# Kernel tuning notes

Measured on AMD Instinct MI355X. Metric: run time of the kernel, lower is better.

The kernel has to match this reference:

```python
import jax, jax.numpy as jnp
import numpy as np

DIM = 1536
HEADS = 12
HD = DIM // HEADS  # 128
EPS = 1e-6
SINK_SIZE = 1          # frames
MAX_ATTN = 1920        # tokens (sliding window)


def setup_inputs() -> dict:
    key = jax.random.key(0)
    ks = jax.random.split(key, 10)
    B = 1
    F, H, W = 8, 16, 24
    L = F * H * W  # 3072
    s = 0.02
    inp = {
        "x": jax.random.normal(ks[0], (B, L, DIM), jnp.float32),
        "seq_lens": jnp.array([L], jnp.int32),
        "grid_sizes": jnp.array([[F, H, W]], jnp.int32),
        "freqs": jax.random.normal(ks[1], (1024, HD // 2, 2), jnp.float32),
        "wq": jax.random.normal(ks[2], (DIM, DIM), jnp.float32) * s,
        "bq": jnp.zeros((DIM,), jnp.float32),
        "wk": jax.random.normal(ks[3], (DIM, DIM), jnp.float32) * s,
        "bk": jnp.zeros((DIM,), jnp.float32),
        "wv": jax.random.normal(ks[4], (DIM, DIM), jnp.float32) * s,
        "bv": jnp.zeros((DIM,), jnp.float32),
        "wo": jax.random.normal(ks[5], (DIM, DIM), jnp.float32) * s,
        "bo": jnp.zeros((DIM,), jnp.float32),
        "nq_w": jnp.ones((DIM,), jnp.float32),
        "nk_w": jnp.ones((DIM,), jnp.float32),
    }
    return inp


def _rmsnorm(x, w):
    # WanRMSNorm: x * rsqrt(mean(x^2) + eps) * weight
    return x * jax.lax.rsqrt(jnp.mean(x * x, axis=-1, keepdims=True) + EPS) * w


def _rope(x, F, H, W, fc):
    # x: [B, L, n, d]; fc: complex [1024, d//2]
    B, L, n, d = x.shape
    c = d // 2
    c1 = c - 2 * (c // 3)  # temporal split
    c2 = c // 3
    f0, f1, f2 = fc[:, :c1], fc[:, c1:c1 + c2], fc[:, c1 + c2:]
    fr = jnp.concatenate([
        jnp.broadcast_to(f0[:F, None, None, :], (F, H, W, c1)),
        jnp.broadcast_to(f1[None, :H, None, :], (F, H, W, c2)),
        jnp.broadcast_to(f2[None, None, :W, :], (F, H, W, c2)),
    ], axis=-1).reshape(L, 1, c)  # [L, 1, c]
    xp = x.reshape(B, L, n, c, 2)
    xc = jax.lax.complex(xp[..., 0], xp[..., 1])  # [B, L, n, c]
    xr = xc * fr[None]
    return jnp.stack([jnp.real(xr), jnp.imag(xr)], axis=-1).reshape(B, L, n, d)


def reference(x, seq_lens, grid_sizes, freqs, wq, bq, wk, bk, wv, bv, wo, bo, nq_w, nk_w):
    B, L, _ = x.shape
    gs = np.asarray(grid_sizes)[0]
    F, H, W = int(gs[0]), int(gs[1]), int(gs[2])
    fs = H * W  # frame_seqlen
    sink = SINK_SIZE * fs

    q = _rmsnorm(x @ wq.T + bq, nq_w).reshape(B, L, HEADS, HD)
    k = _rmsnorm(x @ wk.T + bk, nk_w).reshape(B, L, HEADS, HD)
    v = (x @ wv.T + bv).reshape(B, L, HEADS, HD)

    fc = jax.lax.complex(freqs[..., 0], freqs[..., 1])  # [1024, HD//2]
    q = _rope(q, F, H, W, fc)
    k = _rope(k, F, H, W, fc)

    # sink + windowed frame-causal block mask (flex_attention block_mask)
    idx = jnp.arange(L)
    qf = idx // fs
    kf = idx // fs
    mask = (kf[None, :] <= qf[:, None]) & (
        (idx[None, :] < sink) | (idx[None, :] >= (qf[:, None] + 1) * fs - MAX_ATTN)
    )  # [L, L]

    scale = 1.0 / np.float32(np.sqrt(HD))
    scores = jnp.einsum('bqnd,bknd->bnqk', q, k) * scale
    scores = jnp.where(mask[None, None], scores, jnp.float32(-1e30))
    attn = jax.nn.softmax(scores, axis=-1)
    out = jnp.einsum('bnqk,bknd->bqnd', attn, v).reshape(B, L, DIM)
    return out @ wo.T + bo
```

## Files before the change

kernel.cpp:

```cpp
#include <hip/hip_runtime.h>
#include <stdint.h>

#define DIMC 1536
#define LTOK 3072
#define HEADS 12
#define HD 128
#define FS 384
#define MAXATTN 1920
#define HTOK 1152
#define NHT 1920

typedef __attribute__((ext_vector_type(4))) float f32x4;
typedef __attribute__((ext_vector_type(8))) short bf16x8;

__device__ __forceinline__ unsigned short f2bf(float f) {
  union { float f; unsigned int u; } c; c.f = f;
  unsigned int u = c.u + 0x7fffu + ((c.u >> 16) & 1u);
  return (unsigned short)(u >> 16);
}
__device__ __forceinline__ float bf2f(unsigned short s) {
  union { unsigned int u; float f; } c; c.u = (unsigned int)s << 16; return c.f;
}

__device__ __forceinline__ void dma16(const void* g, void* l) {
  __builtin_amdgcn_global_load_lds(
      (const __attribute__((address_space(1))) unsigned int*)g,
      (__attribute__((address_space(3))) unsigned int*)l, 16, 0, 0);
}

__global__ __launch_bounds__(256)
void cvt_all_k(const float* __restrict__ x, const float* __restrict__ wq,
               const float* __restrict__ wk, const float* __restrict__ wv,
               const float* __restrict__ wo,
               unsigned short* __restrict__ xb, unsigned short* __restrict__ wqb,
               unsigned short* __restrict__ wkb, unsigned short* __restrict__ wvb,
               unsigned short* __restrict__ wob)
{
  const int i = blockIdx.x * 256 + threadIdx.x;
  const int n0 = LTOK * DIMC / 4;
  const int nw = DIMC * DIMC / 4;
  const float* src; unsigned short* dst; int off;
  if (i < n0) { src = x; dst = xb; off = i; }
  else {
    int j = i - n0; int w = j / nw; off = j - w * nw;
    src = (w == 0) ? wq : (w == 1) ? wk : (w == 2) ? wv : wo;
    dst = (w == 0) ? wqb : (w == 1) ? wkb : (w == 2) ? wvb : wob;
  }
  float4 f = ((const float4*)src)[off];
  uint2 o;
  o.x = (unsigned int)f2bf(f.x) | ((unsigned int)f2bf(f.y) << 16);
  o.y = (unsigned int)f2bf(f.z) | ((unsigned int)f2bf(f.w) << 16);
  ((uint2*)dst)[off] = o;
}

template <bool F32OUT>
__global__ __launch_bounds__(256)
void gemm_nt(const unsigned short* __restrict__ A,
             const unsigned short* __restrict__ B0,
             const unsigned short* __restrict__ B1,
             const unsigned short* __restrict__ B2,
             const float* __restrict__ bias0,
             const float* __restrict__ bias1,
             const float* __restrict__ bias2,
             void* __restrict__ o0, void* __restrict__ o1, void* __restrict__ o2)
{
  const int z = blockIdx.z;
  const unsigned short* Bw = (z == 0) ? B0 : (z == 1) ? B1 : B2;
  const float* bias = (z == 0) ? bias0 : (z == 1) ? bias1 : bias2;
  void* outp = (z == 0) ? o0 : (z == 1) ? o1 : o2;

  __shared__ __align__(16) unsigned short lA[128 * 32];
  __shared__ __align__(16) unsigned short lB[128 * 32];

  const int tid = threadIdx.x;
  const int wave = tid >> 6;
  const int lane = tid & 63;
  const int m0 = blockIdx.y * 128;
  const int n0 = blockIdx.x * 128;
  const int wm = (wave >> 1) * 64;
  const int wn = (wave & 1) * 64;

  f32x4 acc[4][4] = {};

  const int srow = tid >> 2;
  const int scol = (tid & 3) * 8;
  const int fr = lane & 15;
  const int fk = (lane >> 4) * 8;

  unsigned short* la0 = &lA[srow * 32 + scol];
  unsigned short* la1 = &lA[(srow + 64) * 32 + scol];
  unsigned short* lb0 = &lB[srow * 32 + scol];
  unsigned short* lb1 = &lB[(srow + 64) * 32 + scol];
  const unsigned short* ga0 = A  + (size_t)(m0 + srow)      * DIMC + scol;
  const unsigned short* ga1 = A  + (size_t)(m0 + srow + 64) * DIMC + scol;
  const unsigned short* gb0 = Bw + (size_t)(n0 + srow)      * DIMC + scol;
  const unsigned short* gb1 = Bw + (size_t)(n0 + srow + 64) * DIMC + scol;

  for (int k0 = 0; k0 < DIMC; k0 += 32) {
    dma16(ga0 + k0, la0);
    dma16(ga1 + k0, la1);
    dma16(gb0 + k0, lb0);
    dma16(gb1 + k0, lb1);
    __syncthreads();

    bf16x8 af[4], bf[4];
#pragma unroll
    for (int i = 0; i < 4; ++i)
      af[i] = *(const bf16x8*)&lA[(wm + i * 16 + fr) * 32 + fk];
#pragma unroll
    for (int j = 0; j < 4; ++j)
      bf[j] = *(const bf16x8*)&lB[(wn + j * 16 + fr) * 32 + fk];
#pragma unroll
    for (int i = 0; i < 4; ++i)
#pragma unroll
      for (int j = 0; j < 4; ++j)
        acc[i][j] = __builtin_amdgcn_mfma_f32_16x16x32_bf16(af[i], bf[j], acc[i][j], 0, 0, 0);
    __syncthreads();
  }

  const int col = lane & 15;
  const int rb = (lane >> 4) * 4;
#pragma unroll
  for (int j = 0; j < 4; ++j) {
    const int gn = n0 + wn + j * 16 + col;
    const float bv = bias[gn];
#pragma unroll
    for (int i = 0; i < 4; ++i) {
#pragma unroll
      for (int r = 0; r < 4; ++r) {
        const int gm = m0 + wm + i * 16 + rb + r;
        float val = acc[i][j][r] + bv;
        if (F32OUT)
          ((float*)outp)[(size_t)gm * DIMC + gn] = val;
        else
          ((unsigned short*)outp)[(size_t)gm * DIMC + gn] = f2bf(val);
      }
    }
  }
}

__global__ __launch_bounds__(256)
void rms_rope_k(unsigned short* __restrict__ q, unsigned short* __restrict__ k,
                const float* __restrict__ nqw, const float* __restrict__ nkw,
                const float* __restrict__ freqs)
{
  const int tok = blockIdx.x;
  const int which = blockIdx.y;
  unsigned short* row = (which ? k : q) + (size_t)tok * DIMC;
  const float* nw = which ? nkw : nqw;
  const float sc = which ? 1.f : (0.08838834764831845f * 1.4426950408889634f);
  const int tid = threadIdx.x;
  const int base = tid * 6;

  float v[6];
  float ss = 0.f;
#pragma unroll
  for (int j = 0; j < 6; ++j) {
    v[j] = bf2f(row[base + j]);
    ss += v[j] * v[j];
  }
#pragma unroll
  for (int off = 1; off < 64; off <<= 1) ss += __shfl_xor(ss, off);
  __shared__ float wsum[4];
  if ((tid & 63) == 0) wsum[tid >> 6] = ss;
  __syncthreads();
  const float total = wsum[0] + wsum[1] + wsum[2] + wsum[3];
  const float rms = rsqrtf(total * (1.f / DIMC) + 1e-6f);

  const int f = tok / FS;
  const int rem = tok - f * FS;
  const int h = rem / 24;
  const int w = rem - h * 24;

#pragma unroll
  for (int pp = 0; pp < 3; ++pp) {
    const int P = (base >> 1) + pp;
    const int p = P & 63;
    const int t = (p < 22) ? f : ((p < 43) ? h : w);
    const float fr = freqs[t * 128 + p * 2];
    const float fi = freqs[t * 128 + p * 2 + 1];
    const float e = v[2 * pp]     * rms * nw[base + 2 * pp];
    const float o = v[2 * pp + 1] * rms * nw[base + 2 * pp + 1];
    row[base + 2 * pp]     = f2bf((e * fr - o * fi) * sc);
    row[base + 2 * pp + 1] = f2bf((e * fi + o * fr) * sc);
  }
}

__global__ __launch_bounds__(256)
void transpose_v_k(const unsigned short* __restrict__ v,
                   unsigned short* __restrict__ vt)
{
  __shared__ __align__(16) unsigned short t[64 * 72];
  const int tb = blockIdx.x * 64;
  const int db = blockIdx.y * 64;
  const int tid = threadIdx.x;
#pragma unroll
  for (int it = 0; it < 2; ++it) {
    int c = tid + it * 256;
    int tok = c >> 3, dc = (c & 7) * 8;
    uint4 val = *(const uint4*)(v + (size_t)(tb + tok) * DIMC + db + dc);
    unsigned short tmp[8];
    *(uint4*)tmp = val;
#pragma unroll
    for (int j = 0; j < 8; ++j) t[(dc + j) * 72 + tok] = tmp[j];
  }
  __syncthreads();
#pragma unroll
  for (int it = 0; it < 2; ++it) {
    int c = tid + it * 256;
    int d = c >> 3, tc = (c & 7) * 8;
    *(uint4*)(vt + ((size_t)db + d) * LTOK + tb + tc) = *(const uint4*)&t[d * 72 + tc];
  }
}

__global__ __launch_bounds__(256, 2)
void attn_flash(const unsigned short* __restrict__ q,
                const unsigned short* __restrict__ k,
                const unsigned short* __restrict__ vt,
                unsigned short* __restrict__ ab,
                float* __restrict__ Opart,
                float* __restrict__ mlbuf)
{
  const int bid = blockIdx.x;
  int qb, head, chunk, nchunks;
  if (bid < 720) { const int hb = bid >> 1; qb = 47 - hb / 12; head = hb % 12; chunk = bid & 1; nchunks = 2; }
  else           { const int lb = bid - 720; qb = 17 - lb / 12; head = lb % 12; chunk = 0; nchunks = 1; }

  const int q0 = qb * 64;
  const int qf = qb / 6;
  const int kend = (qf + 1) * FS;
  const int s2 = kend - MAXATTN;
  const bool two = (s2 > FS);
  const int nt1 = (two ? FS : kend) >> 6;
  const int nt  = nt1 + (two ? (MAXATTN >> 6) : 0);
  const int half = nt / nchunks;
  const int tstart = chunk * half, tend = tstart + half;

  const int tid = threadIdx.x;
  const int wave = tid >> 6, lane = tid & 63;
  const int col = lane & 15;
  const int g = lane >> 4;
  const int g4 = g * 4;

  __shared__ __align__(16) unsigned short Kl[64 * 136];
  __shared__ __align__(16) unsigned short Vtl[128 * 72];
  __shared__ __align__(16) unsigned short Pl[4][16 * 72];

  bf16x8 qfrag[4];
  {
    const unsigned short* qrow = q + (size_t)(q0 + wave * 16 + col) * DIMC + head * HD;
#pragma unroll
    for (int kk = 0; kk < 4; ++kk)
      qfrag[kk] = *(const bf16x8*)(qrow + kk * 32 + g * 8);
  }

  f32x4 oacc[8] = {};
  float m = -3.0e38f, l = 0.f;

  const unsigned short* kgb = k  + (size_t)(tid >> 4) * DIMC + head * HD + (tid & 15) * 8;
  const unsigned short* vgb = vt + ((size_t)head * HD + (tid >> 3)) * LTOK + (tid & 7) * 8;
  unsigned short* kls = &Kl[(tid >> 4) * 136 + (tid & 15) * 8];
  unsigned short* vls = &Vtl[(tid >> 3) * 72 + (tid & 7) * 8];

  uint4 kr0, kr1, kr2, kr3, vr0, vr1, vr2, vr3;
  {
    const int kb = (tstart < nt1) ? tstart * 64 : s2 + (tstart - nt1) * 64;
    const unsigned short* kp = kgb + (size_t)kb * DIMC;
    kr0 = *(const uint4*)(kp);
    kr1 = *(const uint4*)(kp + (size_t)16 * DIMC);
    kr2 = *(const uint4*)(kp + (size_t)32 * DIMC);
    kr3 = *(const uint4*)(kp + (size_t)48 * DIMC);
    const unsigned short* vp = vgb + kb;
    vr0 = *(const uint4*)(vp);
    vr1 = *(const uint4*)(vp + (size_t)32 * LTOK);
    vr2 = *(const uint4*)(vp + (size_t)64 * LTOK);
    vr3 = *(const uint4*)(vp + (size_t)96 * LTOK);
  }

  for (int t = tstart; t < tend; ++t) {
    *(uint4*)(kls)            = kr0;
    *(uint4*)(kls + 16 * 136) = kr1;
    *(uint4*)(kls + 32 * 136) = kr2;
    *(uint4*)(kls + 48 * 136) = kr3;
    *(uint4*)(vls)            = vr0;
    *(uint4*)(vls + 32 * 72)  = vr1;
    *(uint4*)(vls + 64 * 72)  = vr2;
    *(uint4*)(vls + 96 * 72)  = vr3;
    __syncthreads();

    if (t + 1 < tend) {
      const int kb = (t + 1 < nt1) ? (t + 1) * 64 : s2 + (t + 1 - nt1) * 64;
      const unsigned short* kp = kgb + (size_t)kb * DIMC;
      kr0 = *(const uint4*)(kp);
      kr1 = *(const uint4*)(kp + (size_t)16 * DIMC);
      kr2 = *(const uint4*)(kp + (size_t)32 * DIMC);
      kr3 = *(const uint4*)(kp + (size_t)48 * DIMC);
      const unsigned short* vp = vgb + kb;
      vr0 = *(const uint4*)(vp);
      vr1 = *(const uint4*)(vp + (size_t)32 * LTOK);
      vr2 = *(const uint4*)(vp + (size_t)64 * LTOK);
      vr3 = *(const uint4*)(vp + (size_t)96 * LTOK);
    }

    f32x4 s[4] = {};
#pragma unroll
    for (int kt = 0; kt < 4; ++kt)
#pragma unroll
      for (int kk = 0; kk < 4; ++kk) {
        bf16x8 kfr = *(const bf16x8*)&Kl[(kt * 16 + col) * 136 + kk * 32 + g * 8];
        s[kt] = __builtin_amdgcn_mfma_f32_16x16x32_bf16(kfr, qfrag[kk], s[kt], 0, 0, 0);
      }

    float mx = s[0][0];
#pragma unroll
    for (int kt = 0; kt < 4; ++kt)
#pragma unroll
      for (int r = 0; r < 4; ++r) mx = fmaxf(mx, s[kt][r]);
    mx = fmaxf(mx, __shfl_xor(mx, 16));
    mx = fmaxf(mx, __shfl_xor(mx, 32));
    const float mn = fmaxf(m, mx);
    const float al = exp2f(m - mn);
    m = mn;
    float rs = 0.f;
#pragma unroll
    for (int kt = 0; kt < 4; ++kt) {
      const unsigned short p0 = f2bf(exp2f(s[kt][0] - m));
      const unsigned short p1 = f2bf(exp2f(s[kt][1] - m));
      const unsigned short p2 = f2bf(exp2f(s[kt][2] - m));
      const unsigned short p3 = f2bf(exp2f(s[kt][3] - m));
      rs += bf2f(p0) + bf2f(p1) + bf2f(p2) + bf2f(p3);
      uint2 pk;
      pk.x = (unsigned int)p0 | ((unsigned int)p1 << 16);
      pk.y = (unsigned int)p2 | ((unsigned int)p3 << 16);
      *(uint2*)&Pl[wave][col * 72 + kt * 16 + g4] = pk;
    }
    rs += __shfl_xor(rs, 16);
    rs += __shfl_xor(rs, 32);
    l = l * al + rs;
#pragma unroll
    for (int dt = 0; dt < 8; ++dt) oacc[dt] *= al;

#pragma unroll
    for (int step = 0; step < 2; ++step) {
      bf16x8 pf = *(const bf16x8*)&Pl[wave][col * 72 + step * 32 + g * 8];
#pragma unroll
      for (int dt = 0; dt < 8; ++dt) {
        bf16x8 vf = *(const bf16x8*)&Vtl[(dt * 16 + col) * 72 + step * 32 + g * 8];
        oacc[dt] = __builtin_amdgcn_mfma_f32_16x16x32_bf16(vf, pf, oacc[dt], 0, 0, 0);
      }
    }
    __syncthreads();
  }

  if (nchunks == 1) {
    const float linv = 1.f / l;
    unsigned short* orow = ab + (size_t)(q0 + wave * 16 + col) * DIMC + head * HD;
#pragma unroll
    for (int dt = 0; dt < 8; ++dt) {
      uint2 pk;
      pk.x = (unsigned int)f2bf(oacc[dt][0] * linv) | ((unsigned int)f2bf(oacc[dt][1] * linv) << 16);
      pk.y = (unsigned int)f2bf(oacc[dt][2] * linv) | ((unsigned int)f2bf(oacc[dt][3] * linv) << 16);
      *(uint2*)(orow + dt * 16 + g4) = pk;
    }
  } else {
    const int tokp = q0 + wave * 16 + col - HTOK;
    float* ob = Opart + ((size_t)(chunk * NHT + tokp) * HEADS + head) * HD;
#pragma unroll
    for (int dt = 0; dt < 8; ++dt)
      *(f32x4*)(ob + dt * 16 + g4) = oacc[dt];
    if (lane < 16) {
      float* mlp = mlbuf + 2 * ((size_t)(chunk * NHT + tokp) * HEADS + head);
      mlp[0] = m; mlp[1] = l;
    }
  }
}

__global__ __launch_bounds__(384)
void merge_k(const float* __restrict__ Opart, const float* __restrict__ mlbuf,
             unsigned short* __restrict__ ab)
{
  const int tokp = blockIdx.x;
  const int tid = threadIdx.x;
  const int e = tid * 4;
  const int head = e >> 7;
  const size_t r0 = (size_t)tokp * DIMC + e;
  float4 o0 = *(const float4*)(Opart + r0);
  float4 o1 = *(const float4*)(Opart + (size_t)NHT * DIMC + r0);
  const float* ml0 = mlbuf + 2 * ((size_t)tokp * HEADS + head);
  const float* ml1 = mlbuf + 2 * ((size_t)(NHT + tokp) * HEADS + head);
  const float m0 = ml0[0], l0 = ml0[1], m1 = ml1[0], l1 = ml1[1];
  const float mm = fmaxf(m0, m1);
  const float a0 = exp2f(m0 - mm), a1 = exp2f(m1 - mm);
  const float inv = 1.f / (l0 * a0 + l1 * a1);
  uint2 pk;
  pk.x = (unsigned int)f2bf((o0.x * a0 + o1.x * a1) * inv) |
         ((unsigned int)f2bf((o0.y * a0 + o1.y * a1) * inv) << 16);
  pk.y = (unsigned int)f2bf((o0.z * a0 + o1.z * a1) * inv) |
         ((unsigned int)f2bf((o0.w * a0 + o1.w * a1) * inv) << 16);
  *(uint2*)(ab + (size_t)(HTOK + tokp) * DIMC + e) = pk;
}

extern "C" void kernel_launch(void* const* d_in, const int* in_sizes, int n_in,
                              void* d_out, int out_size, void* d_ws, size_t ws_size,
                              hipStream_t stream)
{
  (void)in_sizes; (void)n_in; (void)out_size; (void)ws_size;
  const float* x     = (const float*)d_in[0];
  const float* freqs = (const float*)d_in[3];
  const float* wq    = (const float*)d_in[4];
  const float* bq    = (const float*)d_in[5];
  const float* wk    = (const float*)d_in[6];
  const float* bk    = (const float*)d_in[7];
  const float* wv    = (const float*)d_in[8];
  const float* bv    = (const float*)d_in[9];
  const float* wo    = (const float*)d_in[10];
  const float* bo    = (const float*)d_in[11];
  const float* nqw   = (const float*)d_in[12];
  const float* nkw   = (const float*)d_in[13];

  char* ws = (char*)d_ws;
  size_t off = 0;
  auto take = [&](size_t bytes) -> void* {
    void* p = ws + off; off += (bytes + 255) & ~(size_t)255; return p;
  };
  unsigned short* wob = (unsigned short*)take((size_t)DIMC * DIMC * 2);
  unsigned short* qb  = (unsigned short*)take((size_t)LTOK * DIMC * 2);
  unsigned short* kb  = (unsigned short*)take((size_t)LTOK * DIMC * 2);
  unsigned short* vb  = (unsigned short*)take((size_t)LTOK * DIMC * 2);
  unsigned short* ab  = (unsigned short*)take((size_t)LTOK * DIMC * 2);
  unsigned short* vtb = (unsigned short*)take((size_t)LTOK * DIMC * 2);
  unsigned short* xb  = (unsigned short*)take((size_t)LTOK * DIMC * 2);
  unsigned short* wqb = (unsigned short*)take((size_t)DIMC * DIMC * 2);
  unsigned short* wkb = (unsigned short*)take((size_t)DIMC * DIMC * 2);
  unsigned short* wvb = (unsigned short*)take((size_t)DIMC * DIMC * 2);
  float* mlb = (float*)take((size_t)2 * NHT * HEADS * 2 * sizeof(float));
  float* Opart = (float*)xb;

  cvt_all_k<<<dim3(13824), dim3(256), 0, stream>>>(x, wq, wk, wv, wo,
                                                   xb, wqb, wkb, wvb, wob);

  gemm_nt<false><<<dim3(DIMC / 128, LTOK / 128, 3), dim3(256), 0, stream>>>(
      xb, wqb, wkb, wvb, bq, bk, bv, qb, kb, vb);

  rms_rope_k<<<dim3(LTOK, 2), dim3(256), 0, stream>>>(qb, kb, nqw, nkw, freqs);
  transpose_v_k<<<dim3(LTOK / 64, DIMC / 64), dim3(256), 0, stream>>>(vb, vtb);

  attn_flash<<<dim3(936), dim3(256), 0, stream>>>(qb, kb, vtb, ab, Opart, mlb);
  merge_k<<<dim3(NHT), dim3(384), 0, stream>>>(Opart, mlb, ab);

  gemm_nt<true><<<dim3(DIMC / 128, LTOK / 128, 1), dim3(256), 0, stream>>>(
      ab, wob, wob, wob, bo, bo, bo, d_out, d_out, d_out);
}
```

Baseline: 331.1 us.

## Keep P in registers, widen GEMM to 512 threads, fuse rope and V transpose

The GEMM now uses 512 threads per block. Each wave computes a 32x64 sub-tile, which cuts accumulator registers in half and adds waves per block. The RMSNorm/RoPE and V-transpose kernels merge into one launch, and the transpose writes V columns in a permuted 4-element order. In the attention kernel, the softmax P fragments are packed straight into MFMA operands instead of going through LDS. The permuted V layout is what makes those register fragments line up. The attention occupancy hint is raised from 2 to 4 blocks per CU. The main risks are correctness from the permutation and register pressure under the higher occupancy bound.

```diff
diff --git a/kernel.cpp b/kernel.cpp
--- a/kernel.cpp
+++ b/kernel.cpp
@@ -54,7 +54,7 @@
 }
 
 template <bool F32OUT>
-__global__ __launch_bounds__(256)
+__global__ __launch_bounds__(512)
 void gemm_nt(const unsigned short* __restrict__ A,
              const unsigned short* __restrict__ B0,
              const unsigned short* __restrict__ B1,
@@ -77,41 +77,35 @@
   const int lane = tid & 63;
   const int m0 = blockIdx.y * 128;
   const int n0 = blockIdx.x * 128;
-  const int wm = (wave >> 1) * 64;
+  const int wm = (wave >> 1) * 32;
   const int wn = (wave & 1) * 64;
 
-  f32x4 acc[4][4] = {};
+  f32x4 acc[2][4] = {};
 
   const int srow = tid >> 2;
   const int scol = (tid & 3) * 8;
   const int fr = lane & 15;
   const int fk = (lane >> 4) * 8;
 
-  unsigned short* la0 = &lA[srow * 32 + scol];
-  unsigned short* la1 = &lA[(srow + 64) * 32 + scol];
-  unsigned short* lb0 = &lB[srow * 32 + scol];
-  unsigned short* lb1 = &lB[(srow + 64) * 32 + scol];
-  const unsigned short* ga0 = A  + (size_t)(m0 + srow)      * DIMC + scol;
-  const unsigned short* ga1 = A  + (size_t)(m0 + srow + 64) * DIMC + scol;
-  const unsigned short* gb0 = Bw + (size_t)(n0 + srow)      * DIMC + scol;
-  const unsigned short* gb1 = Bw + (size_t)(n0 + srow + 64) * DIMC + scol;
+  unsigned short* la = &lA[srow * 32 + scol];
+  unsigned short* lb = &lB[srow * 32 + scol];
+  const unsigned short* ga = A  + (size_t)(m0 + srow) * DIMC + scol;
+  const unsigned short* gb = Bw + (size_t)(n0 + srow) * DIMC + scol;
 
   for (int k0 = 0; k0 < DIMC; k0 += 32) {
-    dma16(ga0 + k0, la0);
-    dma16(ga1 + k0, la1);
-    dma16(gb0 + k0, lb0);
-    dma16(gb1 + k0, lb1);
-    __syncthreads();
-
-    bf16x8 af[4], bf[4];
-#pragma unroll
-    for (int i = 0; i < 4; ++i)
+    dma16(ga + k0, la);
+    dma16(gb + k0, lb);
+    __syncthreads();
+
+    bf16x8 af[2], bf[4];
+#pragma unroll
+    for (int i = 0; i < 2; ++i)
       af[i] = *(const bf16x8*)&lA[(wm + i * 16 + fr) * 32 + fk];
 #pragma unroll
     for (int j = 0; j < 4; ++j)
       bf[j] = *(const bf16x8*)&lB[(wn + j * 16 + fr) * 32 + fk];
 #pragma unroll
-    for (int i = 0; i < 4; ++i)
+    for (int i = 0; i < 2; ++i)
 #pragma unroll
       for (int j = 0; j < 4; ++j)
         acc[i][j] = __builtin_amdgcn_mfma_f32_16x16x32_bf16(af[i], bf[j], acc[i][j], 0, 0, 0);
@@ -125,7 +119,7 @@
     const int gn = n0 + wn + j * 16 + col;
     const float bv = bias[gn];
 #pragma unroll
-    for (int i = 0; i < 4; ++i) {
+    for (int i = 0; i < 2; ++i) {
 #pragma unroll
       for (int r = 0; r < 4; ++r) {
         const int gm = m0 + wm + i * 16 + rb + r;
@@ -139,81 +133,85 @@
   }
 }
 
+__device__ __forceinline__ int vperm4(int G) {
+  return (((G >> 3) & 1) << 3) | (((G >> 1) & 1) << 2) | ((G & 1) << 1) | ((G >> 2) & 1);
+}
+
 __global__ __launch_bounds__(256)
-void rms_rope_k(unsigned short* __restrict__ q, unsigned short* __restrict__ k,
+void post_qkv_k(unsigned short* __restrict__ q, unsigned short* __restrict__ k,
+                const unsigned short* __restrict__ v, unsigned short* __restrict__ vt,
                 const float* __restrict__ nqw, const float* __restrict__ nkw,
                 const float* __restrict__ freqs)
 {
-  const int tok = blockIdx.x;
-  const int which = blockIdx.y;
-  unsigned short* row = (which ? k : q) + (size_t)tok * DIMC;
-  const float* nw = which ? nkw : nqw;
-  const float sc = which ? 1.f : (0.08838834764831845f * 1.4426950408889634f);
+  const int bx = blockIdx.x;
   const int tid = threadIdx.x;
-  const int base = tid * 6;
-
-  float v[6];
-  float ss = 0.f;
-#pragma unroll
-  for (int j = 0; j < 6; ++j) {
-    v[j] = bf2f(row[base + j]);
-    ss += v[j] * v[j];
-  }
-#pragma unroll
-  for (int off = 1; off < 64; off <<= 1) ss += __shfl_xor(ss, off);
-  __shared__ float wsum[4];
-  if ((tid & 63) == 0) wsum[tid >> 6] = ss;
-  __syncthreads();
-  const float total = wsum[0] + wsum[1] + wsum[2] + wsum[3];
-  const float rms = rsqrtf(total * (1.f / DIMC) + 1e-6f);
-
-  const int f = tok / FS;
-  const int rem = tok - f * FS;
-  const int h = rem / 24;
-  const int w = rem - h * 24;
-
-#pragma unroll
-  for (int pp = 0; pp < 3; ++pp) {
-    const int P = (base >> 1) + pp;
-    const int p = P & 63;
-    const int t = (p < 22) ? f : ((p < 43) ? h : w);
-    const float fr = freqs[t * 128 + p * 2];
-    const float fi = freqs[t * 128 + p * 2 + 1];
-    const float e = v[2 * pp]     * rms * nw[base + 2 * pp];
-    const float o = v[2 * pp + 1] * rms * nw[base + 2 * pp + 1];
-    row[base + 2 * pp]     = f2bf((e * fr - o * fi) * sc);
-    row[base + 2 * pp + 1] = f2bf((e * fi + o * fr) * sc);
-  }
-}
-
-__global__ __launch_bounds__(256)
-void transpose_v_k(const unsigned short* __restrict__ v,
-                   unsigned short* __restrict__ vt)
-{
-  __shared__ __align__(16) unsigned short t[64 * 72];
-  const int tb = blockIdx.x * 64;
-  const int db = blockIdx.y * 64;
-  const int tid = threadIdx.x;
-#pragma unroll
-  for (int it = 0; it < 2; ++it) {
-    int c = tid + it * 256;
-    int tok = c >> 3, dc = (c & 7) * 8;
-    uint4 val = *(const uint4*)(v + (size_t)(tb + tok) * DIMC + db + dc);
-    unsigned short tmp[8];
-    *(uint4*)tmp = val;
-#pragma unroll
-    for (int j = 0; j < 8; ++j) t[(dc + j) * 72 + tok] = tmp[j];
-  }
-  __syncthreads();
-#pragma unroll
-  for (int it = 0; it < 2; ++it) {
-    int c = tid + it * 256;
-    int d = c >> 3, tc = (c & 7) * 8;
-    *(uint4*)(vt + ((size_t)db + d) * LTOK + tb + tc) = *(const uint4*)&t[d * 72 + tc];
-  }
-}
-
-__global__ __launch_bounds__(256, 2)
+  if (bx < 2 * LTOK) {
+    const int which = bx >= LTOK;
+    const int tok = bx - which * LTOK;
+    unsigned short* row = (which ? k : q) + (size_t)tok * DIMC;
+    const float* nw = which ? nkw : nqw;
+    const float sc = which ? 1.f : (0.08838834764831845f * 1.4426950408889634f);
+    const int base = tid * 6;
+
+    float vv[6];
+    float ss = 0.f;
+#pragma unroll
+    for (int j = 0; j < 6; ++j) {
+      vv[j] = bf2f(row[base + j]);
+      ss += vv[j] * vv[j];
+    }
+#pragma unroll
+    for (int off = 1; off < 64; off <<= 1) ss += __shfl_xor(ss, off);
+    __shared__ float wsum[4];
+    if ((tid & 63) == 0) wsum[tid >> 6] = ss;
+    __syncthreads();
+    const float total = wsum[0] + wsum[1] + wsum[2] + wsum[3];
+    const float rms = rsqrtf(total * (1.f / DIMC) + 1e-6f);
+
+    const int f = tok / FS;
+    const int rem = tok - f * FS;
+    const int h = rem / 24;
+    const int w = rem - h * 24;
+
+#pragma unroll
+    for (int pp = 0; pp < 3; ++pp) {
+      const int P = (base >> 1) + pp;
+      const int p = P & 63;
+      const int t = (p < 22) ? f : ((p < 43) ? h : w);
+      const float fre = freqs[t * 128 + p * 2];
+      const float fim = freqs[t * 128 + p * 2 + 1];
+      const float e = vv[2 * pp]     * rms * nw[base + 2 * pp];
+      const float o = vv[2 * pp + 1] * rms * nw[base + 2 * pp + 1];
+      row[base + 2 * pp]     = f2bf((e * fre - o * fim) * sc);
+      row[base + 2 * pp + 1] = f2bf((e * fim + o * fre) * sc);
+    }
+  } else {
+    const int c0 = bx - 2 * LTOK;
+    const int tb = (c0 % 48) * 64;
+    const int db = (c0 / 48) * 64;
+    __shared__ __align__(16) unsigned short t[64 * 72];
+#pragma unroll
+    for (int it = 0; it < 2; ++it) {
+      int c = tid + it * 256;
+      int tok = c >> 3, dc = (c & 7) * 8;
+      uint4 val = *(const uint4*)(v + (size_t)(tb + tok) * DIMC + db + dc);
+      unsigned short tmp[8];
+      *(uint4*)tmp = val;
+#pragma unroll
+      for (int j = 0; j < 8; ++j) t[(dc + j) * 72 + tok] = tmp[j];
+    }
+    __syncthreads();
+#pragma unroll
+    for (int it = 0; it < 4; ++it) {
+      int c = tid + it * 256;
+      int d = c >> 4, G = c & 15;
+      *(uint2*)(vt + ((size_t)db + d) * LTOK + tb + vperm4(G) * 4) =
+          *(const uint2*)&t[d * 72 + G * 4];
+    }
+  }
+}
+
+__global__ __launch_bounds__(256, 4)
 void attn_flash(const unsigned short* __restrict__ q,
                 const unsigned short* __restrict__ k,
                 const unsigned short* __restrict__ vt,
@@ -244,7 +242,6 @@
 
   __shared__ __align__(16) unsigned short Kl[64 * 136];
   __shared__ __align__(16) unsigned short Vtl[128 * 72];
-  __shared__ __align__(16) unsigned short Pl[4][16 * 72];
 
   bf16x8 qfrag[4];
   {
@@ -322,32 +319,40 @@
     const float al = exp2f(m - mn);
     m = mn;
     float rs = 0.f;
-#pragma unroll
-    for (int kt = 0; kt < 4; ++kt) {
-      const unsigned short p0 = f2bf(exp2f(s[kt][0] - m));
-      const unsigned short p1 = f2bf(exp2f(s[kt][1] - m));
-      const unsigned short p2 = f2bf(exp2f(s[kt][2] - m));
-      const unsigned short p3 = f2bf(exp2f(s[kt][3] - m));
-      rs += bf2f(p0) + bf2f(p1) + bf2f(p2) + bf2f(p3);
-      uint2 pk;
-      pk.x = (unsigned int)p0 | ((unsigned int)p1 << 16);
-      pk.y = (unsigned int)p2 | ((unsigned int)p3 << 16);
-      *(uint2*)&Pl[wave][col * 72 + kt * 16 + g4] = pk;
-    }
+    unsigned int P00, P01, P10, P11, P20, P21, P30, P31;
+#define DOKT(KT, PA, PB)                                      \
+    {                                                         \
+      const unsigned short p0 = f2bf(exp2f(s[KT][0] - m));    \
+      const unsigned short p1 = f2bf(exp2f(s[KT][1] - m));    \
+      const unsigned short p2 = f2bf(exp2f(s[KT][2] - m));    \
+      const unsigned short p3 = f2bf(exp2f(s[KT][3] - m));    \
+      rs += bf2f(p0) + bf2f(p1) + bf2f(p2) + bf2f(p3);        \
+      PA = (unsigned int)p0 | ((unsigned int)p1 << 16);       \
+      PB = (unsigned int)p2 | ((unsigned int)p3 << 16);       \
+    }
+    DOKT(0, P00, P01)
+    DOKT(1, P10, P11)
+    DOKT(2, P20, P21)
+    DOKT(3, P30, P31)
+#undef DOKT
     rs += __shfl_xor(rs, 16);
     rs += __shfl_xor(rs, 32);
     l = l * al + rs;
 #pragma unroll
     for (int dt = 0; dt < 8; ++dt) oacc[dt] *= al;
 
-#pragma unroll
-    for (int step = 0; step < 2; ++step) {
-      bf16x8 pf = *(const bf16x8*)&Pl[wave][col * 72 + step * 32 + g * 8];
-#pragma unroll
-      for (int dt = 0; dt < 8; ++dt) {
-        bf16x8 vf = *(const bf16x8*)&Vtl[(dt * 16 + col) * 72 + step * 32 + g * 8];
-        oacc[dt] = __builtin_amdgcn_mfma_f32_16x16x32_bf16(vf, pf, oacc[dt], 0, 0, 0);
-      }
+    union { uint4 u; bf16x8 v; } pf0, pf1;
+    pf0.u.x = P00; pf0.u.y = P01; pf0.u.z = P10; pf0.u.w = P11;
+    pf1.u.x = P20; pf1.u.y = P21; pf1.u.z = P30; pf1.u.w = P31;
+#pragma unroll
+    for (int dt = 0; dt < 8; ++dt) {
+      bf16x8 vf0 = *(const bf16x8*)&Vtl[(dt * 16 + col) * 72 + g * 8];
+      oacc[dt] = __builtin_amdgcn_mfma_f32_16x16x32_bf16(vf0, pf0.v, oacc[dt], 0, 0, 0);
+    }
+#pragma unroll
+    for (int dt = 0; dt < 8; ++dt) {
+      bf16x8 vf1 = *(const bf16x8*)&Vtl[(dt * 16 + col) * 72 + 32 + g * 8];
+      oacc[dt] = __builtin_amdgcn_mfma_f32_16x16x32_bf16(vf1, pf1.v, oacc[dt], 0, 0, 0);
     }
     __syncthreads();
   }
@@ -439,15 +444,15 @@
   cvt_all_k<<<dim3(13824), dim3(256), 0, stream>>>(x, wq, wk, wv, wo,
                                                    xb, wqb, wkb, wvb, wob);
 
-  gemm_nt<false><<<dim3(DIMC / 128, LTOK / 128, 3), dim3(256), 0, stream>>>(
+  gemm_nt<false><<<dim3(DIMC / 128, LTOK / 128, 3), dim3(512), 0, stream>>>(
       xb, wqb, wkb, wvb, bq, bk, bv, qb, kb, vb);
 
-  rms_rope_k<<<dim3(LTOK, 2), dim3(256), 0, stream>>>(qb, kb, nqw, nkw, freqs);
-  transpose_v_k<<<dim3(LTOK / 64, DIMC / 64), dim3(256), 0, stream>>>(vb, vtb);
+  post_qkv_k<<<dim3(2 * LTOK + 1152), dim3(256), 0, stream>>>(
+      qb, kb, vb, vtb, nqw, nkw, freqs);
 
   attn_flash<<<dim3(936), dim3(256), 0, stream>>>(qb, kb, vtb, ab, Opart, mlb);
   merge_k<<<dim3(NHT), dim3(384), 0, stream>>>(Opart, mlb, ab);
 
-  gemm_nt<true><<<dim3(DIMC / 128, LTOK / 128, 1), dim3(256), 0, stream>>>(
+  gemm_nt<true><<<dim3(DIMC / 128, LTOK / 128, 1), dim3(512), 0, stream>>>(
       ab, wob, wob, wob, bo, bo, bo, d_out, d_out, d_out);
 }
```

Result: slower. 341.7 us (+3.2%).
